# Optimization experiments

Hardware: AMD Instinct MI355X
Metric: run time of the kernel (lower is better)

The kernel has to match this reference:

```python
import jax, jax.numpy as jnp
import numpy as np

B, N, D = 2, 2048, 1536
HEADS, KVH, DQK, DV = 8, 1, 128, 192
G = HEADS // KVH  # query groups per kv head
NP, DP = 512, 128  # pairwise seq len (coarse), pairwise feature dim
SCALE = DQK ** -0.5
CLAMP = 5.0
MOMENTUM = 0.1  # BatchRMSNorm: 1 - 0.9
EPS = 1e-5


def layernorm(x, w, b):
    mu = jnp.mean(x, axis=-1, keepdims=True)
    var = jnp.mean(jnp.square(x - mu), axis=-1, keepdims=True)
    return (x - mu) * jax.lax.rsqrt(var + EPS) * w + b


def setup_inputs() -> dict:
    key = jax.random.key(0)
    ks = jax.random.split(key, 6)
    w = lambda k, shape: jax.random.normal(k, shape, jnp.float32) * 0.02
    return {
        "x": jax.random.normal(ks[0], (B, N, D), jnp.float32),
        "pairwise": jax.random.normal(ks[1], (B, NP, NP, DP), jnp.float32),
        "w_qkv": w(ks[2], (D, HEADS * DQK + KVH * DQK + KVH * DV)),
        "q_w": jnp.ones((DQK,), jnp.float32), "q_b": jnp.zeros((DQK,), jnp.float32),
        "k_w": jnp.ones((DQK,), jnp.float32), "k_b": jnp.zeros((DQK,), jnp.float32),
        "v_w": jnp.ones((DV,), jnp.float32), "v_b": jnp.zeros((DV,), jnp.float32),
        "bias_gamma": jnp.ones((DP,), jnp.float32),
        "bias_beta": jnp.zeros((DP,), jnp.float32),
        "bias_running_var": jnp.ones((DP,), jnp.float32),
        "w_bias": w(ks[3], (DP, HEADS)),
        "w_out": w(ks[4], (HEADS * DV, D)),
        "b_out": jnp.zeros((D,), jnp.float32),
    }


def reference(x, pairwise, w_qkv, q_w, q_b, k_w, k_b, v_w, v_b,
              bias_gamma, bias_beta, bias_running_var, w_bias, w_out, b_out):
    b, n, _ = x.shape
    qkv = x @ w_qkv
    q, k, v = jnp.split(qkv, [HEADS * DQK, HEADS * DQK + KVH * DQK], axis=-1)
    # split heads: q -> b g h n d, k/v -> b h n d
    q = q.reshape(b, n, G, KVH, DQK).transpose(0, 2, 3, 1, 4)
    k = k.reshape(b, n, KVH, DQK).transpose(0, 2, 1, 3)
    v = v.reshape(b, n, KVH, DV).transpose(0, 2, 1, 3)
    q = layernorm(q, q_w, q_b)
    k = layernorm(k, k_w, k_b)
    v = layernorm(v, v_w, v_b)

    sim = jnp.einsum('bghid,bhjd->bghij', q, k) * SCALE

    # BatchRMSNorm (training update of running_var, then normalize)
    flat = pairwise.reshape(-1, DP)
    batch_var = jnp.var(flat, axis=0)  # unbiased=False
    rv = bias_running_var * (1.0 - MOMENTUM) + MOMENTUM * batch_var
    std = jnp.sqrt(rv + EPS)
    normed = pairwise / std * bias_gamma + bias_beta
    bias = jax.nn.gelu(normed, approximate=False) @ w_bias  # b i j (g h)
    bias = bias.reshape(b, NP, NP, G, KVH).transpose(0, 3, 4, 1, 2)  # b g h i j
    r = n // NP  # expand_factor
    bias = jnp.repeat(jnp.repeat(bias, r, axis=-2), r, axis=-1)

    sim = jnp.tanh((sim + bias) / CLAMP) * CLAMP  # softclamp
    attn = jax.nn.softmax(sim, axis=-1)
    out = jnp.einsum('bghij,bhjd->bghid', attn, v)
    out = out.transpose(0, 3, 1, 2, 4).reshape(b, n, HEADS * DV)  # merge heads
    return out @ w_out + b_out
```

## Files before the change

kernel.cpp:

```cpp
#include <hip/hip_runtime.h>
#include <math.h>

typedef _Float16 f16;
typedef unsigned int u32;
typedef __attribute__((ext_vector_type(8))) f16 f16x8;
typedef __attribute__((ext_vector_type(4))) f16 f16x4;
typedef __attribute__((ext_vector_type(4))) float f32x4;
typedef __attribute__((ext_vector_type(16))) float f32x16;

#define DEV static __device__ __forceinline__

#define SEQ 2048
#define DMODEL 1536
#define NHEADS 8
#define DQK 128
#define DVV 192
#define QKVW 1344
#define SCALEQK 0.08838834764831845f
#define LOG2E 1.4426950408889634f

#define OFF_WQKVT 0ull
#define OFF_WOUTT 4128768ull
#define OFF_QKV   8847360ull
#define OFF_Q     30867456ull
#define OFF_K     39256064ull
#define OFF_V     40304640ull
#define OFF_VT    41877504ull
#define OFF_PART  43450368ull
#define OFF_SG    43712512ull
#define OFF_BIASC 43713536ull
#define OFF_AO    52102144ull

DEV float fexp2(float x){
#if __has_builtin(__builtin_amdgcn_exp2f)
  return __builtin_amdgcn_exp2f(x);
#else
  return exp2f(x);
#endif
}
DEV float frcp(float x){
#if __has_builtin(__builtin_amdgcn_rcpf)
  return __builtin_amdgcn_rcpf(x);
#else
  return 1.0f/x;
#endif
}

typedef u32 __attribute__((address_space(1))) u32g;
typedef u32 __attribute__((address_space(3))) u32l;
DEV void g2l16(const void* g, void* l){
  __builtin_amdgcn_global_load_lds((const u32g*)g, (u32l*)l, 16, 0, 0);
}

#define MFMA32(a,b,c) __builtin_amdgcn_mfma_f32_32x32x16_f16(a,b,c,0,0,0)
#define MFMA16(a,b,c) __builtin_amdgcn_mfma_f32_16x16x32_f16(a,b,c,0,0,0)

DEV f32x16 zero16(){
  f32x16 v;
  #pragma unroll
  for (int i=0;i<16;i++) v[i]=0.f;
  return v;
}
DEV f32x4 zero4(){
  f32x4 v;
  #pragma unroll
  for (int i=0;i<4;i++) v[i]=0.f;
  return v;
}
DEV float gelu_f(float x){ return 0.5f*x*(1.f + erff(x*0.70710678118654752440f)); }

__global__ __launch_bounds__(256) void k1_wtrans(const float* __restrict__ wq, f16* __restrict__ wqT,
                                                 const float* __restrict__ wo, f16* __restrict__ woT){
  __shared__ float t[32][33];
  int bid = blockIdx.x, tid = threadIdx.x;
  int tx = tid & 31, ty = tid >> 5;
  const float* src; f16* dst; int N, x, y;
  if (bid < 2016){ src = wq; dst = wqT; N = 1344; x = bid % 48; y = bid / 48; }
  else { int b2 = bid - 2016; src = wo; dst = woT; N = 1536; x = b2 % 48; y = b2 / 48; }
  int k0 = x*32, n0 = y*32;
  #pragma unroll
  for (int i=0;i<4;i++){ int r = ty+8*i; t[r][tx] = src[(size_t)(k0+r)*N + n0+tx]; }
  __syncthreads();
  #pragma unroll
  for (int i=0;i<4;i++){ int r = ty+8*i; dst[(size_t)(n0+r)*1536 + k0+tx] = (f16)t[tx][r]; }
}

DEV void qkv_body(const float* __restrict__ X, const f16* __restrict__ WT,
                  float* __restrict__ qkv, char* lds, int bx, int by, int tid){
  int nb = bx*64, mb = by*128;
  int w = tid>>6, lane = tid&63, li = lane&31, h = lane>>5;
  int arow = tid>>4, acq = tid&15;
  int brow = lane>>3, bc = lane&7;
  f32x16 acc[2]; acc[0]=zero16(); acc[1]=zero16();
  f32x4 ar[8];

#define QG_ISSUE_B(buf, kt_) do { \
    char* bd = lds + (buf)*24576 + 16384; \
    _Pragma("unroll") \
    for (int s=0;s<2;s++){ \
      int slot = w*2+s; int nl = slot*8 + brow; int cs = bc ^ (nl&7); \
      g2l16(WT + (size_t)(nb+nl)*DMODEL + (kt_)*64 + cs*8, bd + slot*1024); \
    } } while(0)
#define QG_LOAD_A(kt_) do { \
    _Pragma("unroll") \
    for (int i=0;i<8;i++) \
      ar[i] = *(const f32x4*)(X + (size_t)(mb + arow + 16*i)*DMODEL + (kt_)*64 + acq*4); \
    } while(0)
#define QG_WRITE_A(buf) do { \
    char* ad = lds + (buf)*24576; \
    _Pragma("unroll") \
    for (int i=0;i<8;i++){ \
      int rr = arow + 16*i; int ch = (acq>>1) ^ (rr&7); \
      f16x4 t4; t4[0]=(f16)ar[i][0]; t4[1]=(f16)ar[i][1]; t4[2]=(f16)ar[i][2]; t4[3]=(f16)ar[i][3]; \
      *(f16x4*)(ad + rr*128 + ch*16 + (acq&1)*8) = t4; \
    } } while(0)

  QG_ISSUE_B(0,0); QG_LOAD_A(0); QG_WRITE_A(0);
  __syncthreads();
  for (int kt=0; kt<24; kt++){
    int cur = kt&1;
    if (kt<23){ QG_ISSUE_B(cur^1, kt+1); QG_LOAD_A(kt+1); }
    const char* ad = lds + cur*24576;
    const char* bd = lds + cur*24576 + 16384;
    int ml = w*32 + li;
    #pragma unroll
    for (int ks=0; ks<4; ks++){
      f16x8 af = *(const f16x8*)(ad + ml*128 + (((2*ks+h) ^ (ml&7))*16));
      #pragma unroll
      for (int nf=0; nf<2; nf++){
        int nl = nf*32 + li;
        f16x8 bf = *(const f16x8*)(bd + nl*128 + (((2*ks+h) ^ (nl&7))*16));
        acc[nf] = MFMA32(af, bf, acc[nf]);
      }
    }
    if (kt<23) QG_WRITE_A(cur^1);
    __syncthreads();
  }
  #pragma unroll
  for (int nf=0; nf<2; nf++)
    #pragma unroll
    for (int r=0;r<16;r++){
      int m = mb + w*32 + (r&3) + 8*(r>>2) + 4*h;
      int n = nb + nf*32 + li;
      qkv[(size_t)m*QKVW + n] = acc[nf][r];
    }
#undef QG_ISSUE_B
#undef QG_LOAD_A
#undef QG_WRITE_A
}

DEV void pvar_body(const float* __restrict__ pw, float* __restrict__ partials,
                   char* smem, int id, int tid){
  int c = tid & 127, hh = tid >> 7;
  float s1 = 0.f, s2 = 0.f;
  const float* p0 = pw + ((size_t)id*2048 + hh)*128 + c;
  #pragma unroll 8
  for (int it=0; it<1024; it++){
    float v = p0[(size_t)it*256];
    s1 += v; s2 += v*v;
  }
  float* r1 = (float*)smem; float* r2 = r1 + 256;
  r1[tid] = s1; r2[tid] = s2;
  __syncthreads();
  if (tid < 128){
    partials[(size_t)id*256 + tid]       = r1[tid] + r1[tid+128];
    partials[(size_t)id*256 + 128 + tid] = r2[tid] + r2[tid+128];
  }
}

__global__ __launch_bounds__(256,2) void k2_qkv_pvar(const float* __restrict__ X,
    const f16* __restrict__ WT, float* __restrict__ qkv,
    const float* __restrict__ pw, float* __restrict__ partials){
  __shared__ char smem[49152];
  int bid = blockIdx.x, tid = threadIdx.x;
  if (bid < 512){
    if ((bid & 1) == 0){ int qid = bid>>1; qkv_body(X, WT, qkv, smem, qid%21, qid/21, tid); }
    else               { pvar_body(pw, partials, smem, bid>>1, tid); }
  } else {
    int qid = 256 + (bid - 512);
    qkv_body(X, WT, qkv, smem, qid%21, qid/21, tid);
  }
}

DEV void ln_unit(const float* __restrict__ qkv,
    const float* __restrict__ qw, const float* __restrict__ qb,
    const float* __restrict__ kw, const float* __restrict__ kb,
    const float* __restrict__ vw, const float* __restrict__ vb,
    f16* __restrict__ Q, f16* __restrict__ K, f16* __restrict__ V,
    int unit, int lane){
  int row = unit / 10, seg = unit - row*10;
  int b = row >> 11, n = row & 2047;
  const float* base = qkv + (size_t)row*QKVW;
  if (seg < 9){
    int off = seg*128;
    float x0 = base[off+lane], x1 = base[off+64+lane];
    float s = x0+x1;
    #pragma unroll
    for (int d=32; d>=1; d>>=1) s += __shfl_xor(s, d);
    float mu = s*(1.f/128.f);
    float d0 = x0-mu, d1 = x1-mu;
    float vv = d0*d0 + d1*d1;
    #pragma unroll
    for (int d=32; d>=1; d>>=1) vv += __shfl_xor(vv, d);
    float istd = rsqrtf(vv*(1.f/128.f) + 1e-5f);
    const float* W  = (seg<8)? qw : kw;
    const float* Bi = (seg<8)? qb : kb;
    f16* dst = (seg<8) ? (Q + ((size_t)(b*NHEADS+seg)*SEQ + n)*DQK)
                       : (K + ((size_t)(b*SEQ+n))*DQK);
    dst[lane]    = (f16)(d0*istd*W[lane] + Bi[lane]);
    dst[lane+64] = (f16)(d1*istd*W[lane+64] + Bi[lane+64]);
  } else {
    float x0 = base[1152+lane], x1 = base[1152+64+lane], x2 = base[1152+128+lane];
    float s = x0+x1+x2;
    #pragma unroll
    for (int d=32; d>=1; d>>=1) s += __shfl_xor(s, d);
    float mu = s*(1.f/192.f);
    float d0=x0-mu, d1=x1-mu, d2=x2-mu;
    float vv = d0*d0+d1*d1+d2*d2;
    #pragma unroll
    for (int d=32; d>=1; d>>=1) vv += __shfl_xor(vv, d);
    float istd = rsqrtf(vv*(1.f/192.f) + 1e-5f);
    f16* dst = V + (size_t)(b*SEQ+n)*DVV;
    dst[lane]     = (f16)(d0*istd*vw[lane] + vb[lane]);
    dst[lane+64]  = (f16)(d1*istd*vw[lane+64] + vb[lane+64]);
    dst[lane+128] = (f16)(d2*istd*vw[lane+128] + vb[lane+128]);
  }
}

__global__ __launch_bounds__(256,4) void k3_ln_finvar(const float* __restrict__ qkv,
    const float* __restrict__ qw, const float* __restrict__ qb,
    const float* __restrict__ kw, const float* __restrict__ kb,
    const float* __restrict__ vw, const float* __restrict__ vb,
    f16* __restrict__ Q, f16* __restrict__ K, f16* __restrict__ V,
    const float* __restrict__ partials, const float* __restrict__ rvar,
    const float* __restrict__ gamma, const float* __restrict__ beta,
    float* __restrict__ sg, float* __restrict__ sb){
  __shared__ float sh[256];
  int bid = blockIdx.x, tid = threadIdx.x;
  if (bid < 10240){
    ln_unit(qkv, qw,qb,kw,kb,vw,vb, Q,K,V, bid*4 + (tid>>6), tid&63);
  } else {
    int c = tid & 127, wh = tid >> 7;
    float acc = 0.f;
    #pragma unroll 4
    for (int i=0;i<256;i++) acc += partials[i*256 + wh*128 + c];
    sh[tid] = acc;
    __syncthreads();
    if (tid < 128){
      float s1 = sh[tid], s2 = sh[tid+128];
      const float Minv = 1.f/524288.f;
      float m = s1*Minv;
      float var = s2*Minv - m*m;
      float rv = rvar[tid]*0.9f + 0.1f*var;
      sg[tid] = rsqrtf(rv + 1e-5f)*gamma[tid];
      sb[tid] = beta[tid];
    }
  }
}

DEV void bias_body(const float* __restrict__ pw,
    const float* __restrict__ sg, const float* __restrict__ sb,
    const float* __restrict__ wb, f16* __restrict__ biasc, int bias_id, int tid){
  int w = tid>>6, lane = tid&63;
  int il = lane&15, kg = lane>>4;
  f16x8 bw[4];
  float sgr[32], sbr[32];
  #pragma unroll
  for (int t=0;t<4;t++)
    #pragma unroll
    for (int e=0;e<8;e++){
      int k = t*32 + kg*8 + e;
      bw[t][e] = (f16)((il<8) ? wb[k*8 + il] : 0.f);
      sgr[t*8+e] = sg[k];
      sbr[t*8+e] = sb[k];
    }
  for (int it=0; it<8; it++){
    int tile = bias_id*4 + w + it*4096;
    size_t rg = (size_t)tile*16 + il;
    f32x4 acc = zero4();
    #pragma unroll
    for (int t=0;t<4;t++){
      const float* sp = pw + rg*128 + t*32 + kg*8;
      f32x4 v0 = *(const f32x4*)sp;
      f32x4 v1 = *(const f32x4*)(sp+4);
      f16x8 af;
      #pragma unroll
      for (int e=0;e<4;e++) af[e]   = (f16)gelu_f(v0[e]*sgr[t*8+e]   + sbr[t*8+e]);
      #pragma unroll
      for (int e=0;e<4;e++) af[4+e] = (f16)gelu_f(v1[e]*sgr[t*8+4+e] + sbr[t*8+4+e]);
      acc = MFMA16(af, bw[t], acc);
    }
    if (il < 8){
      #pragma unroll
      for (int r=0;r<4;r++){
        size_t rr = (size_t)tile*16 + kg*4 + r;
        int bb = (int)(rr >> 18);
        int rem = (int)(rr & 262143);
        int ii = rem >> 9, jj = rem & 511;
        biasc[(((size_t)(bb*8 + il)*512) + ii)*512 + jj] = (f16)acc[r];
      }
    }
  }
}

DEV void vtrans_body(const f16* __restrict__ V, f16* __restrict__ VT,
                     f16 (*t)[33], int id, int tid){
  int b = id / 384, rem = id - b*384;
  int d0 = (rem % 6)*32, j0 = (rem / 6)*32;
  int tx = tid & 31, ty = tid >> 5;
  #pragma unroll
  for (int i=0;i<4;i++){ int r = ty+8*i; t[r][tx] = V[((size_t)b*SEQ + j0+r)*DVV + d0+tx]; }
  __syncthreads();
  #pragma unroll
  for (int i=0;i<4;i++){ int r = ty+8*i; VT[((size_t)b*DVV + d0+r)*SEQ + j0+tx] = t[tx][r]; }
}

__global__ __launch_bounds__(256,2) void k4_bias_vtrans(const float* __restrict__ pw,
    const float* __restrict__ sg, const float* __restrict__ sb,
    const float* __restrict__ wb, f16* __restrict__ biasc,
    const f16* __restrict__ V, f16* __restrict__ VT){
  __shared__ f16 tt[32][33];
  int bid = blockIdx.x, tid = threadIdx.x;
  if (bid < 1536){
    if (bid & 1) bias_body(pw, sg, sb, wb, biasc, bid>>1, tid);
    else         vtrans_body(V, VT, tt, bid>>1, tid);
  } else {
    bias_body(pw, sg, sb, wb, biasc, 768 + (bid - 1536), tid);
  }
}

__global__ __launch_bounds__(256,1) void attn(const f16* __restrict__ Q, const f16* __restrict__ K,
                                              const f16* __restrict__ VT, const f16* __restrict__ biasc,
                                              f16* __restrict__ AO){
  __shared__ char lds[81920];
  int bid = blockIdx.x;
  int bg = bid & 15, qt = bid >> 4;
  int b = bg >> 3, g = bg & 7;
  int tid = threadIdx.x;
  int w = tid >> 6, lane = tid & 63;
  int li = lane & 31, h = lane >> 5;

  const f16* Qb = Q  + (size_t)bg*SEQ*DQK;
  const f16* Kb = K  + (size_t)b*SEQ*DQK;
  const f16* Vb = VT + (size_t)b*DVV*SEQ;

  int qrow = qt*128 + w*32 + li;
  f16x8 qf[8];
  #pragma unroll
  for (int ks=0; ks<8; ks++)
    qf[ks] = *(const f16x8*)(Qb + (size_t)qrow*DQK + ks*16 + h*8);

  const f16* brow = biasc + ((size_t)bg*512 + (qrow>>2))*512;

  f32x16 oacc[6];
  #pragma unroll
  for (int nf=0;nf<6;nf++) oacc[nf] = zero16();
  float lsum = 0.f;

  int kl_row = lane >> 4, kl_c = lane & 15;
  int vl_row = lane >> 3, vl_c = lane & 7;

#define STAGE(buf, jt_) do { \
    char* kd = lds + (buf)*40960; \
    const f16* ksrc = Kb + (size_t)(jt_)*64*DQK; \
    _Pragma("unroll") \
    for (int s=0;s<4;s++){ \
      int slot = w*4+s; int jr = slot*4 + kl_row; int cs = kl_c ^ (jr&7); \
      g2l16(ksrc + (size_t)jr*DQK + cs*8, kd + slot*1024); \
    } \
    char* vd = lds + (buf)*40960 + 16384; \
    _Pragma("unroll") \
    for (int s=0;s<6;s++){ \
      int slot = w*6+s; int dvr = slot*8 + vl_row; int cs = vl_c ^ (dvr&7); \
      g2l16(Vb + (size_t)dvr*SEQ + (size_t)(jt_)*64 + cs*8, vd + slot*1024); \
    } } while(0)

  STAGE(0, 0);

  const float CS = SCALEQK * (2.f*LOG2E/5.f);
  const float CB = 2.f*LOG2E/5.f;
  const float CP = 5.f*LOG2E;

  for (int jt=0; jt<32; jt++){
    int cur = jt & 1;
    __syncthreads();
    if (jt < 31) STAGE(cur^1, jt+1);
    const char* kb_ = lds + cur*40960;
    const char* vb_ = lds + cur*40960 + 16384;
    #pragma unroll
    for (int sub=0; sub<2; sub++){
      f32x16 sacc = zero16();
      int jr = sub*32 + li;
      __builtin_amdgcn_s_setprio(1);
      #pragma unroll
      for (int ks=0; ks<8; ks++){
        int ck = (2*ks + h) ^ (jr&7);
        f16x8 kf = *(const f16x8*)(kb_ + jr*256 + ck*16);
        sacc = MFMA32(kf, qf[ks], sacc);
      }
      __builtin_amdgcn_s_setprio(0);
      int jb4 = jt*16 + sub*8;
      f16x8 bv = *(const f16x8*)(brow + jb4);
      float bt[4];
      #pragma unroll
      for (int q=0;q<4;q++){
        float b0 = (float)bv[2*q], b1 = (float)bv[2*q+1];
        bt[q] = (h ? b1 : b0) * CB;
      }
      float p[16], xp[16];
      #pragma unroll
      for (int r=0;r<16;r++){
        float u2 = sacc[r]*CS + bt[r>>2];
        float E  = fexp2(u2);
        float tn = 1.f - 2.f*frcp(E + 1.f);
        float pr = fexp2(tn * CP);
        p[r] = pr;
        lsum += pr;
      }
      #pragma unroll
      for (int r=0;r<16;r++) xp[r] = __shfl_xor(p[r], 32);
      __builtin_amdgcn_s_setprio(1);
      #pragma unroll
      for (int ks2=0; ks2<2; ks2++){
        f16x8 pa;
        #pragma unroll
        for (int e=0;e<4;e++) pa[e] = (f16)(h ? xp[8*ks2+4+e] : p[8*ks2+e]);
        #pragma unroll
        for (int e=4;e<8;e++) pa[e] = (f16)(h ? p[8*ks2+e]    : xp[8*ks2+e-4]);
        #pragma unroll
        for (int nf=0; nf<6; nf++){
          int dvr = nf*32 + li;
          int cj = (sub*4 + 2*ks2 + h) ^ (dvr&7);
          f16x8 vf = *(const f16x8*)(vb_ + dvr*128 + cj*16);
          oacc[nf] = MFMA32(pa, vf, oacc[nf]);
        }
      }
      __builtin_amdgcn_s_setprio(0);
    }
  }
  float ltot = lsum + __shfl_xor(lsum, 32);
  float linv = 1.f / ltot;
  #pragma unroll
  for (int nf=0; nf<6; nf++)
    #pragma unroll
    for (int r=0;r<16;r++){
      int il = (r&3) + 8*(r>>2) + 4*h;
      float ov = oacc[nf][r] * __shfl(linv, il);
      int orow = qt*128 + w*32 + il;
      AO[((size_t)(b*SEQ + orow)*NHEADS + g)*DVV + nf*32 + li] = (f16)ov;
    }
#undef STAGE
}

__global__ __launch_bounds__(256,2) void out_gemm(const f16* __restrict__ A, const f16* __restrict__ WT,
                                                  const float* __restrict__ bo, float* __restrict__ out){
  __shared__ char lds[49152];
  int nb = blockIdx.x*64, mb = blockIdx.y*128;
  int tid = threadIdx.x;
  int w = tid>>6, lane = tid&63, li = lane&31, h = lane>>5;
  int srow = lane>>3, sc = lane&7;
  f32x16 acc[2]; acc[0]=zero16(); acc[1]=zero16();

#define OG_STAGE(buf, kt_) do { \
    char* ad = lds + (buf)*24576; \
    _Pragma("unroll") \
    for (int s=0;s<4;s++){ \
      int slot = w*4+s; int mlr = slot*8 + srow; int cs = sc ^ (mlr&7); \
      g2l16(A + (size_t)(mb+mlr)*DMODEL + (kt_)*64 + cs*8, ad + slot*1024); \
    } \
    char* bd = lds + (buf)*24576 + 16384; \
    _Pragma("unroll") \
    for (int s=0;s<2;s++){ \
      int slot = w*2+s; int nl = slot*8 + srow; int cs = sc ^ (nl&7); \
      g2l16(WT + (size_t)(nb+nl)*DMODEL + (kt_)*64 + cs*8, bd + slot*1024); \
    } } while(0)

  OG_STAGE(0,0);
  __syncthreads();
  for (int kt=0; kt<24; kt++){
    int cur = kt&1;
    if (kt<23) OG_STAGE(cur^1, kt+1);
    const char* ad = lds + cur*24576;
    const char* bd = lds + cur*24576 + 16384;
    int ml = w*32 + li;
    #pragma unroll
    for (int ks=0; ks<4; ks++){
      f16x8 af = *(const f16x8*)(ad + ml*128 + (((2*ks+h) ^ (ml&7))*16));
      #pragma unroll
      for (int nf=0; nf<2; nf++){
        int nl = nf*32 + li;
        f16x8 bf = *(const f16x8*)(bd + nl*128 + (((2*ks+h) ^ (nl&7))*16));
        acc[nf] = MFMA32(af, bf, acc[nf]);
      }
    }
    __syncthreads();
  }
  float bo0 = bo[nb+li], bo1 = bo[nb+32+li];
  #pragma unroll
  for (int nf=0; nf<2; nf++)
    #pragma unroll
    for (int r=0;r<16;r++){
      int m = mb + w*32 + (r&3) + 8*(r>>2) + 4*h;
      int n = nb + nf*32 + li;
      out[(size_t)m*DMODEL + n] = acc[nf][r] + (nf ? bo1 : bo0);
    }
#undef OG_STAGE
}

extern "C" void kernel_launch(void* const* d_in, const int* in_sizes, int n_in,
                              void* d_out, int out_size, void* d_ws, size_t ws_size,
                              hipStream_t stream) {
  (void)in_sizes; (void)n_in; (void)out_size; (void)ws_size;
  const float* x        = (const float*)d_in[0];
  const float* pairwise = (const float*)d_in[1];
  const float* w_qkv    = (const float*)d_in[2];
  const float* q_w      = (const float*)d_in[3];
  const float* q_b      = (const float*)d_in[4];
  const float* k_w      = (const float*)d_in[5];
  const float* k_b      = (const float*)d_in[6];
  const float* v_w      = (const float*)d_in[7];
  const float* v_b      = (const float*)d_in[8];
  const float* bgamma   = (const float*)d_in[9];
  const float* bbeta    = (const float*)d_in[10];
  const float* brvar    = (const float*)d_in[11];
  const float* w_bias   = (const float*)d_in[12];
  const float* w_out    = (const float*)d_in[13];
  const float* b_out    = (const float*)d_in[14];
  float* out = (float*)d_out;

  char* ws = (char*)d_ws;
  f16*   wqkvT = (f16*)(ws + OFF_WQKVT);
  f16*   woutT = (f16*)(ws + OFF_WOUTT);
  float* qkvb  = (float*)(ws + OFF_QKV);
  f16*   Qh    = (f16*)(ws + OFF_Q);
  f16*   Kh    = (f16*)(ws + OFF_K);
  f16*   Vh    = (f16*)(ws + OFF_V);
  f16*   VTh   = (f16*)(ws + OFF_VT);
  float* part  = (float*)(ws + OFF_PART);
  float* sg    = (float*)(ws + OFF_SG);
  float* sb    = sg + 128;
  f16*   biasc = (f16*)(ws + OFF_BIASC);
  f16*   AOh   = (f16*)(ws + OFF_AO);

  k1_wtrans<<<4320, 256, 0, stream>>>(w_qkv, wqkvT, w_out, woutT);
  k2_qkv_pvar<<<928, 256, 0, stream>>>(x, wqkvT, qkvb, pairwise, part);
  k3_ln_finvar<<<10241, 256, 0, stream>>>(qkvb, q_w,q_b,k_w,k_b,v_w,v_b, Qh, Kh, Vh,
                                          part, brvar, bgamma, bbeta, sg, sb);
  k4_bias_vtrans<<<1792, 256, 0, stream>>>(pairwise, sg, sb, w_bias, biasc, Vh, VTh);
  attn<<<256, 256, 0, stream>>>(Qh, Kh, VTh, biasc, AOh);
  out_gemm<<<dim3(24,32), 256, 0, stream>>>(AOh, woutT, b_out, out);
}
```

Measured before the change: 384.9 us.

## Pre-convert X to fp16, async-stage A tiles, vectorize pvar, approximate GELU

```diff
diff --git a/kernel.cpp b/kernel.cpp
--- a/kernel.cpp
+++ b/kernel.cpp
@@ -21,15 +21,16 @@
 
 #define OFF_WQKVT 0ull
 #define OFF_WOUTT 4128768ull
-#define OFF_QKV   8847360ull
-#define OFF_Q     30867456ull
-#define OFF_K     39256064ull
-#define OFF_V     40304640ull
-#define OFF_VT    41877504ull
-#define OFF_PART  43450368ull
-#define OFF_SG    43712512ull
-#define OFF_BIASC 43713536ull
-#define OFF_AO    52102144ull
+#define OFF_XH    8847360ull
+#define OFF_QKV   21430272ull
+#define OFF_Q     43450368ull
+#define OFF_K     51838976ull
+#define OFF_V     52887552ull
+#define OFF_VT    54460416ull
+#define OFF_PART  56033280ull
+#define OFF_SG    57081856ull
+#define OFF_BIASC 57082880ull
+#define OFF_AO    65471488ull
 
 DEV float fexp2(float x){
 #if __has_builtin(__builtin_amdgcn_exp2f)
@@ -67,12 +68,33 @@
   for (int i=0;i<4;i++) v[i]=0.f;
   return v;
 }
-DEV float gelu_f(float x){ return 0.5f*x*(1.f + erff(x*0.70710678118654752440f)); }
-
-__global__ __launch_bounds__(256) void k1_wtrans(const float* __restrict__ wq, f16* __restrict__ wqT,
-                                                 const float* __restrict__ wo, f16* __restrict__ woT){
+
+DEV float gelu_f(float x){
+  float z  = 0.70710678118654752440f * x;
+  float az = fabsf(z);
+  float t  = frcp(1.f + 0.3275911f*az);
+  float poly = t*(0.254829592f + t*(-0.284496736f + t*(1.421413741f +
+               t*(-1.453152027f + t*1.061405429f))));
+  float e  = 1.f - poly*fexp2(-z*z*LOG2E);
+  float er = (z < 0.f) ? -e : e;
+  return 0.5f*x*(1.f + er);
+}
+
+__global__ __launch_bounds__(256) void k1_prep(const float* __restrict__ wq, f16* __restrict__ wqT,
+                                               const float* __restrict__ wo, f16* __restrict__ woT,
+                                               const float* __restrict__ X, f16* __restrict__ Xh){
   __shared__ float t[32][33];
   int bid = blockIdx.x, tid = threadIdx.x;
+  if (bid >= 4320){
+    size_t i0 = (size_t)(bid - 4320)*2048 + (size_t)tid*8;
+    f32x4 a = *(const f32x4*)(X + i0);
+    f32x4 b = *(const f32x4*)(X + i0 + 4);
+    f16x8 o;
+    #pragma unroll
+    for (int e=0;e<4;e++){ o[e] = (f16)a[e]; o[4+e] = (f16)b[e]; }
+    *(f16x8*)(Xh + i0) = o;
+    return;
+  }
   int tx = tid & 31, ty = tid >> 5;
   const float* src; f16* dst; int N, x, y;
   if (bid < 2016){ src = wq; dst = wqT; N = 1344; x = bid % 48; y = bid / 48; }
@@ -85,41 +107,32 @@
   for (int i=0;i<4;i++){ int r = ty+8*i; dst[(size_t)(n0+r)*1536 + k0+tx] = (f16)t[tx][r]; }
 }
 
-DEV void qkv_body(const float* __restrict__ X, const f16* __restrict__ WT,
+DEV void qkv_body(const f16* __restrict__ A, const f16* __restrict__ WT,
                   float* __restrict__ qkv, char* lds, int bx, int by, int tid){
   int nb = bx*64, mb = by*128;
   int w = tid>>6, lane = tid&63, li = lane&31, h = lane>>5;
-  int arow = tid>>4, acq = tid&15;
-  int brow = lane>>3, bc = lane&7;
+  int srow = lane>>3, sc = lane&7;
   f32x16 acc[2]; acc[0]=zero16(); acc[1]=zero16();
-  f32x4 ar[8];
-
-#define QG_ISSUE_B(buf, kt_) do { \
+
+#define QG_STAGE(buf, kt_) do { \
+    char* ad = lds + (buf)*24576; \
+    _Pragma("unroll") \
+    for (int s=0;s<4;s++){ \
+      int slot = w*4+s; int mlr = slot*8 + srow; int cs = sc ^ (mlr&7); \
+      g2l16(A + (size_t)(mb+mlr)*DMODEL + (kt_)*64 + cs*8, ad + slot*1024); \
+    } \
     char* bd = lds + (buf)*24576 + 16384; \
     _Pragma("unroll") \
     for (int s=0;s<2;s++){ \
-      int slot = w*2+s; int nl = slot*8 + brow; int cs = bc ^ (nl&7); \
+      int slot = w*2+s; int nl = slot*8 + srow; int cs = sc ^ (nl&7); \
       g2l16(WT + (size_t)(nb+nl)*DMODEL + (kt_)*64 + cs*8, bd + slot*1024); \
     } } while(0)
-#define QG_LOAD_A(kt_) do { \
-    _Pragma("unroll") \
-    for (int i=0;i<8;i++) \
-      ar[i] = *(const f32x4*)(X + (size_t)(mb + arow + 16*i)*DMODEL + (kt_)*64 + acq*4); \
-    } while(0)
-#define QG_WRITE_A(buf) do { \
-    char* ad = lds + (buf)*24576; \
-    _Pragma("unroll") \
-    for (int i=0;i<8;i++){ \
-      int rr = arow + 16*i; int ch = (acq>>1) ^ (rr&7); \
-      f16x4 t4; t4[0]=(f16)ar[i][0]; t4[1]=(f16)ar[i][1]; t4[2]=(f16)ar[i][2]; t4[3]=(f16)ar[i][3]; \
-      *(f16x4*)(ad + rr*128 + ch*16 + (acq&1)*8) = t4; \
-    } } while(0)
-
-  QG_ISSUE_B(0,0); QG_LOAD_A(0); QG_WRITE_A(0);
+
+  QG_STAGE(0,0);
   __syncthreads();
   for (int kt=0; kt<24; kt++){
     int cur = kt&1;
-    if (kt<23){ QG_ISSUE_B(cur^1, kt+1); QG_LOAD_A(kt+1); }
+    if (kt<23) QG_STAGE(cur^1, kt+1);
     const char* ad = lds + cur*24576;
     const char* bd = lds + cur*24576 + 16384;
     int ml = w*32 + li;
@@ -133,7 +146,6 @@
         acc[nf] = MFMA32(af, bf, acc[nf]);
       }
     }
-    if (kt<23) QG_WRITE_A(cur^1);
     __syncthreads();
   }
   #pragma unroll
@@ -144,41 +156,43 @@
       int n = nb + nf*32 + li;
       qkv[(size_t)m*QKVW + n] = acc[nf][r];
     }
-#undef QG_ISSUE_B
-#undef QG_LOAD_A
-#undef QG_WRITE_A
+#undef QG_STAGE
 }
 
 DEV void pvar_body(const float* __restrict__ pw, float* __restrict__ partials,
                    char* smem, int id, int tid){
-  int c = tid & 127, hh = tid >> 7;
-  float s1 = 0.f, s2 = 0.f;
-  const float* p0 = pw + ((size_t)id*2048 + hh)*128 + c;
-  #pragma unroll 8
-  for (int it=0; it<1024; it++){
-    float v = p0[(size_t)it*256];
+  int q = tid & 31, rg = tid >> 5;
+  f32x4 s1 = zero4(), s2 = zero4();
+  const float* p0 = pw + ((size_t)id*512 + rg)*128 + q*4;
+  #pragma unroll 4
+  for (int it=0; it<64; it++){
+    f32x4 v = *(const f32x4*)(p0 + (size_t)it*1024);
     s1 += v; s2 += v*v;
   }
-  float* r1 = (float*)smem; float* r2 = r1 + 256;
+  f32x4* r1 = (f32x4*)smem; f32x4* r2 = r1 + 256;
   r1[tid] = s1; r2[tid] = s2;
   __syncthreads();
-  if (tid < 128){
-    partials[(size_t)id*256 + tid]       = r1[tid] + r1[tid+128];
-    partials[(size_t)id*256 + 128 + tid] = r2[tid] + r2[tid+128];
-  }
-}
-
-__global__ __launch_bounds__(256,2) void k2_qkv_pvar(const float* __restrict__ X,
+  if (tid < 64){
+    int qq = tid & 31;
+    f32x4* rr = (tid >= 32) ? r2 : r1;
+    f32x4 a = rr[qq];
+    #pragma unroll
+    for (int g=1; g<8; g++) a += rr[g*32+qq];
+    *(f32x4*)(partials + (size_t)id*256 + ((tid>=32)?128:0) + qq*4) = a;
+  }
+}
+
+__global__ __launch_bounds__(256,2) void k2_qkv_pvar(const f16* __restrict__ Xh,
     const f16* __restrict__ WT, float* __restrict__ qkv,
     const float* __restrict__ pw, float* __restrict__ partials){
   __shared__ char smem[49152];
   int bid = blockIdx.x, tid = threadIdx.x;
-  if (bid < 512){
-    if ((bid & 1) == 0){ int qid = bid>>1; qkv_body(X, WT, qkv, smem, qid%21, qid/21, tid); }
-    else               { pvar_body(pw, partials, smem, bid>>1, tid); }
+  if (bid < 1536){
+    if (bid % 3 == 0){ int qid = bid/3; qkv_body(Xh, WT, qkv, smem, qid%21, qid/21, tid); }
+    else { int pid = (bid/3)*2 + (bid%3) - 1; pvar_body(pw, partials, smem, pid, tid); }
   } else {
-    int qid = 256 + (bid - 512);
-    qkv_body(X, WT, qkv, smem, qid%21, qid/21, tid);
+    int qid = 512 + (bid - 1536);
+    qkv_body(Xh, WT, qkv, smem, qid%21, qid/21, tid);
   }
 }
 
@@ -242,8 +256,8 @@
   } else {
     int c = tid & 127, wh = tid >> 7;
     float acc = 0.f;
-    #pragma unroll 4
-    for (int i=0;i<256;i++) acc += partials[i*256 + wh*128 + c];
+    #pragma unroll 8
+    for (int i=0;i<1024;i++) acc += partials[i*256 + wh*128 + c];
     sh[tid] = acc;
     __syncthreads();
     if (tid < 128){
@@ -391,14 +405,12 @@
     for (int sub=0; sub<2; sub++){
       f32x16 sacc = zero16();
       int jr = sub*32 + li;
-      __builtin_amdgcn_s_setprio(1);
       #pragma unroll
       for (int ks=0; ks<8; ks++){
         int ck = (2*ks + h) ^ (jr&7);
         f16x8 kf = *(const f16x8*)(kb_ + jr*256 + ck*16);
         sacc = MFMA32(kf, qf[ks], sacc);
       }
-      __builtin_amdgcn_s_setprio(0);
       int jb4 = jt*16 + sub*8;
       f16x8 bv = *(const f16x8*)(brow + jb4);
       float bt[4];
@@ -419,7 +431,6 @@
       }
       #pragma unroll
       for (int r=0;r<16;r++) xp[r] = __shfl_xor(p[r], 32);
-      __builtin_amdgcn_s_setprio(1);
       #pragma unroll
       for (int ks2=0; ks2<2; ks2++){
         f16x8 pa;
@@ -435,7 +446,6 @@
           oacc[nf] = MFMA32(pa, vf, oacc[nf]);
         }
       }
-      __builtin_amdgcn_s_setprio(0);
     }
   }
   float ltot = lsum + __shfl_xor(lsum, 32);
@@ -531,6 +541,7 @@
   char* ws = (char*)d_ws;
   f16*   wqkvT = (f16*)(ws + OFF_WQKVT);
   f16*   woutT = (f16*)(ws + OFF_WOUTT);
+  f16*   Xh    = (f16*)(ws + OFF_XH);
   float* qkvb  = (float*)(ws + OFF_QKV);
   f16*   Qh    = (f16*)(ws + OFF_Q);
   f16*   Kh    = (f16*)(ws + OFF_K);
@@ -542,8 +553,8 @@
   f16*   biasc = (f16*)(ws + OFF_BIASC);
   f16*   AOh   = (f16*)(ws + OFF_AO);
 
-  k1_wtrans<<<4320, 256, 0, stream>>>(w_qkv, wqkvT, w_out, woutT);
-  k2_qkv_pvar<<<928, 256, 0, stream>>>(x, wqkvT, qkvb, pairwise, part);
+  k1_prep<<<7392, 256, 0, stream>>>(w_qkv, wqkvT, w_out, woutT, x, Xh);
+  k2_qkv_pvar<<<1696, 256, 0, stream>>>(Xh, wqkvT, qkvb, pairwise, part);
   k3_ln_finvar<<<10241, 256, 0, stream>>>(qkvb, q_w,q_b,k_w,k_b,v_w,v_b, Qh, Kh, Vh,
                                           part, brvar, bgamma, bbeta, sg, sb);
   k4_bias_vtrans<<<1792, 256, 0, stream>>>(pairwise, sg, sb, w_bias, biasc, Vh, VTh);
```

Result: faster. 351.3 us (-8.7%).
